# Kernel optimization log

Hardware: AMD Instinct MI355X
Metric: run time of the kernel (lower is better)

## Reference

```python
import jax, jax.numpy as jnp
import numpy as np


def setup_inputs() -> dict:
    key = jax.random.key(0)
    k1, k2, k3, k4 = jax.random.split(key, 4)
    B, L, R, H, D = 64, 512, 512, 512, 256
    return {
        "lstm_lt": jax.random.normal(k1, (B, L, H), dtype=jnp.float32),
        "lstm_rt": jax.random.normal(k2, (B, R, H), dtype=jnp.float32),
        "atten_W": jax.random.normal(k3, (H, D), dtype=jnp.float32) * 0.05,
        "diagnoal_W": jax.random.normal(k4, (1, 1, D), dtype=jnp.float32) * 0.05,
    }


def reference(lstm_lt, lstm_rt, atten_W, diagnoal_W):
    # Projection (the original's broadcast-multiply-sum is exactly a GEMM):
    # atten_lt[b,l,d] = tanh(sum_h lstm_lt[b,l,h] * W[h,d]) * diag_W[d]
    atten_lt = jnp.tanh(jnp.einsum('blh,hd->bld', lstm_lt, atten_W)) * diagnoal_W
    atten_rt = jnp.tanh(jnp.einsum('brh,hd->brd', lstm_rt, atten_W))
    # batch_dot over the attention dim -> (B, L, R)
    atten_value = jnp.einsum('bld,brd->blr', atten_lt, atten_rt)
    # No masks supplied (len(inputs)==2 path); softmax over last axis.
    return jax.nn.softmax(atten_value, axis=-1)
```

## Files before the change

kernel.cpp:

```cpp
#include <hip/hip_runtime.h>

typedef __attribute__((ext_vector_type(8))) __bf16 bf16x8;
typedef __attribute__((ext_vector_type(4))) float f32x4;

#define DI __device__ __forceinline__

DI unsigned short f2bf(float x) {
  unsigned u = __float_as_uint(x);
  u += 0x7fffu + ((u >> 16) & 1u);
  return (unsigned short)(u >> 16);
}

DI bf16x8 cvt8(f32x4 lo, f32x4 hi) {
  bf16x8 r;
  r[0] = (__bf16)lo.x; r[1] = (__bf16)lo.y; r[2] = (__bf16)lo.z; r[3] = (__bf16)lo.w;
  r[4] = (__bf16)hi.x; r[5] = (__bf16)hi.y; r[6] = (__bf16)hi.z; r[7] = (__bf16)hi.w;
  return r;
}

DI float tanh_fast(float x) {
  float ax = fabsf(x);
  float e = __expf(-2.0f * ax);
  float t = (1.0f - e) / (1.0f + e);
  return x < 0.0f ? -t : t;
}


__global__ void k_wt(const float* __restrict__ W, unsigned short* __restrict__ Wt) {
  int n  = blockIdx.x;
  int k8 = threadIdx.x;
  unsigned v[8];
#pragma unroll
  for (int j = 0; j < 8; j++) v[j] = f2bf(W[(k8 * 8 + j) * 256 + n]);
  uint4 p;
  p.x = v[0] | (v[1] << 16);
  p.y = v[2] | (v[3] << 16);
  p.z = v[4] | (v[5] << 16);
  p.w = v[6] | (v[7] << 16);
  size_t idx = ((size_t)(n >> 4) * 16 + (k8 >> 2)) * 512 + (k8 & 3) * 128 + (n & 15) * 8;
  *(uint4*)&Wt[idx] = p;
}

__global__ __launch_bounds__(512, 2) void k_proj(
    const float* __restrict__ Alt, const float* __restrict__ Art,
    const unsigned short* __restrict__ Wt, const float* __restrict__ diag,
    unsigned short* __restrict__ Olt, unsigned short* __restrict__ Ort) {
  int bx = blockIdx.x;
  bool is_lt = bx < 256;
  int m0 = (is_lt ? bx : bx - 256) * 128;
  const char* Abase = (const char*)((is_lt ? Alt : Art) + (size_t)m0 * 512);
  const char* Bt = (const char*)Wt;
  unsigned short* O = is_lt ? Olt : Ort;

  int tid  = threadIdx.x;
  int lane = tid & 63;
  int wid  = tid >> 6;
  int wm   = wid >> 2;
  int wn   = wid & 3;
  int l15  = lane & 15;
  int quad = lane >> 4;

  f32x4 zero = {0.0f, 0.0f, 0.0f, 0.0f};
  f32x4 acc[4][4];
#pragma unroll
  for (int i = 0; i < 4; i++)
#pragma unroll
    for (int j = 0; j < 4; j++) acc[i][j] = zero;

  const char* Arow = Abase + (size_t)(wm * 64 + l15) * 2048 + quad * 32;

#pragma unroll 2
  for (int t = 0; t < 8; t++) {
    uint4 bv[2][4];
#pragma unroll
    for (int ks = 0; ks < 2; ks++)
#pragma unroll
      for (int nt = 0; nt < 4; nt++)
        bv[ks][nt] = *(const uint4*)(
            Bt + (((size_t)(wn * 4 + nt) * 16 + t * 2 + ks) << 10) + lane * 16);

    bf16x8 a[2][4];
#pragma unroll
    for (int ks = 0; ks < 2; ks++)
#pragma unroll
      for (int mt = 0; mt < 4; mt++) {
        const char* ap = Arow + (size_t)mt * 32768 + t * 256 + ks * 128;
        f32x4 lo = *(const f32x4*)(ap);
        f32x4 hi = *(const f32x4*)(ap + 16);
        a[ks][mt] = cvt8(lo, hi);
      }

#pragma unroll
    for (int ks = 0; ks < 2; ks++)
#pragma unroll
      for (int mt = 0; mt < 4; mt++)
#pragma unroll
        for (int nt = 0; nt < 4; nt++)
          acc[mt][nt] = __builtin_amdgcn_mfma_f32_16x16x32_bf16(
              a[ks][mt], __builtin_bit_cast(bf16x8, bv[ks][nt]), acc[mt][nt], 0, 0, 0);
  }

  float dscale[4];
#pragma unroll
  for (int nt = 0; nt < 4; nt++)
    dscale[nt] = is_lt ? diag[wn * 64 + nt * 16 + l15] : 1.0f;

#pragma unroll
  for (int mt = 0; mt < 4; mt++)
#pragma unroll
    for (int r = 0; r < 4; r++) {
      int m = m0 + wm * 64 + mt * 16 + quad * 4 + r;
      int bb = m >> 9, rr = m & 511;
#pragma unroll
      for (int nt = 0; nt < 4; nt++) {
        int d = wn * 64 + nt * 16 + l15;
        size_t idx = (size_t)bb * 131072 +
                     ((size_t)(rr >> 4) * 8 + (d >> 5)) * 512 +
                     ((d >> 3) & 3) * 128 + (rr & 15) * 8 + (d & 7);
        O[idx] = f2bf(tanh_fast(acc[mt][nt][r]) * dscale[nt]);
      }
    }
}

__global__ __launch_bounds__(512, 4) void k_attn(
    const unsigned short* __restrict__ Lt, const unsigned short* __restrict__ Rt,
    float* __restrict__ Out) {
  __shared__ float red[8][64];
  __shared__ float rowv[64];

  int bx = blockIdx.x;
  int b  = (bx & 7) * 8 + ((bx >> 3) & 7);
  int l0 = (bx >> 6) * 64;
  const char* Lb = (const char*)Lt + (size_t)b * 262144;
  const char* Rb = (const char*)Rt + (size_t)b * 262144;
  float* Ob = Out + ((size_t)b * 512 + l0) * 512;

  int tid  = threadIdx.x;
  int lane = tid & 63;
  int wid  = tid >> 6;
  int l15  = lane & 15;
  int quad = lane >> 4;

  f32x4 zero = {0.0f, 0.0f, 0.0f, 0.0f};
  f32x4 acc[4][4];
#pragma unroll
  for (int i = 0; i < 4; i++)
#pragma unroll
    for (int j = 0; j < 4; j++) acc[i][j] = zero;

  int lrow = l0 >> 4;

  for (int t = 0; t < 8; t++) {
    uint4 av[4], rv[4];
#pragma unroll
    for (int mt = 0; mt < 4; mt++)
      av[mt] = *(const uint4*)(Lb + (((size_t)(lrow + mt) * 8 + t) << 10) + lane * 16);
#pragma unroll
    for (int nt = 0; nt < 4; nt++)
      rv[nt] = *(const uint4*)(Rb + (((size_t)(wid * 4 + nt) * 8 + t) << 10) + lane * 16);
#pragma unroll
    for (int mt = 0; mt < 4; mt++)
#pragma unroll
      for (int nt = 0; nt < 4; nt++)
        acc[mt][nt] = __builtin_amdgcn_mfma_f32_16x16x32_bf16(
            __builtin_bit_cast(bf16x8, av[mt]),
            __builtin_bit_cast(bf16x8, rv[nt]), acc[mt][nt], 0, 0, 0);
  }

#pragma unroll
  for (int mt = 0; mt < 4; mt++) {
#pragma unroll
    for (int r = 0; r < 4; r++) {
      float m = fmaxf(fmaxf(acc[mt][0][r], acc[mt][1][r]),
                      fmaxf(acc[mt][2][r], acc[mt][3][r]));
      m = fmaxf(m, __shfl_xor(m, 1));
      m = fmaxf(m, __shfl_xor(m, 2));
      m = fmaxf(m, __shfl_xor(m, 4));
      m = fmaxf(m, __shfl_xor(m, 8));
      if (l15 == 0) red[wid][mt * 16 + quad * 4 + r] = m;
    }
  }
  __syncthreads();
  if (tid < 64) {
    float m = red[0][tid];
#pragma unroll
    for (int w = 1; w < 8; w++) m = fmaxf(m, red[w][tid]);
    rowv[tid] = m;
  }
  __syncthreads();

#pragma unroll
  for (int mt = 0; mt < 4; mt++) {
#pragma unroll
    for (int r = 0; r < 4; r++) {
      float base = rowv[mt * 16 + quad * 4 + r];
      float s = 0.0f;
#pragma unroll
      for (int nt = 0; nt < 4; nt++) {
        float e = __expf(acc[mt][nt][r] - base);
        acc[mt][nt][r] = e;
        s += e;
      }
      s += __shfl_xor(s, 1);
      s += __shfl_xor(s, 2);
      s += __shfl_xor(s, 4);
      s += __shfl_xor(s, 8);
      if (l15 == 0) red[wid][mt * 16 + quad * 4 + r] = s;
    }
  }
  __syncthreads();
  if (tid < 64) {
    float s = red[0][tid];
#pragma unroll
    for (int w = 1; w < 8; w++) s += red[w][tid];
    rowv[tid] = 1.0f / s;
  }
  __syncthreads();

#pragma unroll
  for (int mt = 0; mt < 4; mt++) {
#pragma unroll
    for (int r = 0; r < 4; r++) {
      int row = mt * 16 + quad * 4 + r;
      float inv = rowv[row];
#pragma unroll
      for (int nt = 0; nt < 4; nt++) {
        int col = wid * 64 + nt * 16 + l15;
        Ob[(size_t)row * 512 + col] = acc[mt][nt][r] * inv;
      }
    }
  }
}

extern "C" void kernel_launch(void* const* d_in, const int* in_sizes, int n_in,
                              void* d_out, int out_size, void* d_ws, size_t ws_size,
                              hipStream_t stream) {
  const float* lstm_lt = (const float*)d_in[0];
  const float* lstm_rt = (const float*)d_in[1];
  const float* W       = (const float*)d_in[2];
  const float* diag    = (const float*)d_in[3];
  float* out = (float*)d_out;

  unsigned short* Wt  = (unsigned short*)d_ws;
  unsigned short* Olt = (unsigned short*)((char*)d_ws + (size_t)256 * 512 * 2);
  unsigned short* Ort = Olt + (size_t)32768 * 256;

  k_wt<<<dim3(256), dim3(64), 0, stream>>>(W, Wt);
  k_proj<<<dim3(512), dim3(512), 0, stream>>>(lstm_lt, lstm_rt, Wt, diag, Olt, Ort);
  k_attn<<<dim3(512), dim3(512), 0, stream>>>(Olt, Ort, out);
}
```

Before: 257.7 us.

## Stage projection A tiles through swizzled LDS with double-buffered prefetch

The projection kernel now covers 256 rows per block instead of 128. Each block cooperatively loads fp32 A rows with coalesced loads, converts them to bf16 and stores them in an XOR-swizzled, double-buffered LDS tile. Global loads for the next K step are issued before compute and barriers, so they overlap with the MFMA work, and MFMA sections run at raised wave priority. The cost is twice the accumulator registers (8x4 tiles), 64KB of LDS, and half as many blocks, which may reduce occupancy and latency hiding.

```diff
diff --git a/kernel.cpp b/kernel.cpp
--- a/kernel.cpp
+++ b/kernel.cpp
@@ -23,6 +23,17 @@
   float e = __expf(-2.0f * ax);
   float t = (1.0f - e) / (1.0f + e);
   return x < 0.0f ? -t : t;
+}
+
+DI void barx() {
+  __builtin_amdgcn_sched_barrier(0);
+  __builtin_amdgcn_s_barrier();
+  __builtin_amdgcn_sched_barrier(0);
+}
+DI void lgkm0() {
+  __builtin_amdgcn_sched_barrier(0);
+  asm volatile("s_waitcnt lgkmcnt(0)" ::: "memory");
+  __builtin_amdgcn_sched_barrier(0);
 }
 
 
@@ -45,9 +56,11 @@
     const float* __restrict__ Alt, const float* __restrict__ Art,
     const unsigned short* __restrict__ Wt, const float* __restrict__ diag,
     unsigned short* __restrict__ Olt, unsigned short* __restrict__ Ort) {
+  __shared__ __align__(16) unsigned short As[2][256 * 64];
+
   int bx = blockIdx.x;
-  bool is_lt = bx < 256;
-  int m0 = (is_lt ? bx : bx - 256) * 128;
+  bool is_lt = bx < 128;
+  int m0 = (is_lt ? bx : bx - 128) * 256;
   const char* Abase = (const char*)((is_lt ? Alt : Art) + (size_t)m0 * 512);
   const char* Bt = (const char*)Wt;
   unsigned short* O = is_lt ? Olt : Ort;
@@ -59,45 +72,87 @@
   int wn   = wid & 3;
   int l15  = lane & 15;
   int quad = lane >> 4;
+  int r7   = l15 & 7;
+
+  int srow  = tid >> 1;
+  int soff  = (tid & 1) * 128;
+  int cbase = (tid & 1) * 4;
 
   f32x4 zero = {0.0f, 0.0f, 0.0f, 0.0f};
-  f32x4 acc[4][4];
-#pragma unroll
-  for (int i = 0; i < 4; i++)
+  f32x4 acc[8][4];
+#pragma unroll
+  for (int i = 0; i < 8; i++)
 #pragma unroll
     for (int j = 0; j < 4; j++) acc[i][j] = zero;
 
-  const char* Arow = Abase + (size_t)(wm * 64 + l15) * 2048 + quad * 32;
-
-#pragma unroll 2
-  for (int t = 0; t < 8; t++) {
-    uint4 bv[2][4];
+  f32x4 av[8];
+  uint4 b0[2][4], b1[2][4];
+
+  auto issueA = [&](int t) {
+    const char* ap = Abase + (size_t)srow * 2048 + t * 256 + soff;
+#pragma unroll
+    for (int i = 0; i < 8; i++) av[i] = *(const f32x4*)(ap + i * 16);
+  };
+  auto issueB = [&](int t, uint4 (&b)[2][4]) {
 #pragma unroll
     for (int ks = 0; ks < 2; ks++)
 #pragma unroll
       for (int nt = 0; nt < 4; nt++)
-        bv[ks][nt] = *(const uint4*)(
+        b[ks][nt] = *(const uint4*)(
             Bt + (((size_t)(wn * 4 + nt) * 16 + t * 2 + ks) << 10) + lane * 16);
-
-    bf16x8 a[2][4];
-#pragma unroll
-    for (int ks = 0; ks < 2; ks++)
-#pragma unroll
-      for (int mt = 0; mt < 4; mt++) {
-        const char* ap = Arow + (size_t)mt * 32768 + t * 256 + ks * 128;
-        f32x4 lo = *(const f32x4*)(ap);
-        f32x4 hi = *(const f32x4*)(ap + 16);
-        a[ks][mt] = cvt8(lo, hi);
+  };
+  auto writeA = [&](int buf) {
+    char* AsB = (char*)&As[buf][0];
+#pragma unroll
+    for (int i = 0; i < 4; i++) {
+      int c = cbase + i;
+      *(bf16x8*)(AsB + srow * 128 + ((c ^ (srow & 7)) << 4)) =
+          cvt8(av[i * 2], av[i * 2 + 1]);
+    }
+  };
+  auto compute = [&](int buf, uint4 (&b)[2][4]) {
+    const char* AsB = (const char*)&As[buf][0];
+#pragma unroll
+    for (int ks = 0; ks < 2; ks++) {
+      bf16x8 a[8];
+#pragma unroll
+      for (int mt = 0; mt < 8; mt++) {
+        int row = wm * 128 + mt * 16 + l15;
+        a[mt] = *(const bf16x8*)(AsB + row * 128 + (((ks * 4 + quad) ^ r7) << 4));
       }
-
-#pragma unroll
-    for (int ks = 0; ks < 2; ks++)
-#pragma unroll
-      for (int mt = 0; mt < 4; mt++)
+      __builtin_amdgcn_s_setprio(1);
+#pragma unroll
+      for (int mt = 0; mt < 8; mt++)
 #pragma unroll
         for (int nt = 0; nt < 4; nt++)
           acc[mt][nt] = __builtin_amdgcn_mfma_f32_16x16x32_bf16(
-              a[ks][mt], __builtin_bit_cast(bf16x8, bv[ks][nt]), acc[mt][nt], 0, 0, 0);
+              a[mt], __builtin_bit_cast(bf16x8, b[ks][nt]), acc[mt][nt], 0, 0, 0);
+      __builtin_amdgcn_s_setprio(0);
+    }
+  };
+
+  issueA(0);
+  issueB(0, b0);
+  writeA(0);
+  issueA(1);
+  issueB(1, b1);
+  lgkm0();
+  barx();
+
+#pragma unroll
+  for (int t = 0; t < 8; t += 2) {
+    compute(0, b0);
+    writeA(1);
+    if (t < 6) { issueA(t + 2); issueB(t + 2, b0); }
+    lgkm0();
+    barx();
+    compute(1, b1);
+    if (t < 6) {
+      writeA(0);
+      issueA(t + 3); issueB(t + 3, b1);
+      lgkm0();
+      barx();
+    }
   }
 
   float dscale[4];
@@ -106,10 +161,10 @@
     dscale[nt] = is_lt ? diag[wn * 64 + nt * 16 + l15] : 1.0f;
 
 #pragma unroll
-  for (int mt = 0; mt < 4; mt++)
+  for (int mt = 0; mt < 8; mt++)
 #pragma unroll
     for (int r = 0; r < 4; r++) {
-      int m = m0 + wm * 64 + mt * 16 + quad * 4 + r;
+      int m = m0 + wm * 128 + mt * 16 + quad * 4 + r;
       int bb = m >> 9, rr = m & 511;
 #pragma unroll
       for (int nt = 0; nt < 4; nt++) {
@@ -246,6 +301,6 @@
   unsigned short* Ort = Olt + (size_t)32768 * 256;
 
   k_wt<<<dim3(256), dim3(64), 0, stream>>>(W, Wt);
-  k_proj<<<dim3(512), dim3(512), 0, stream>>>(lstm_lt, lstm_rt, Wt, diag, Olt, Ort);
+  k_proj<<<dim3(256), dim3(512), 0, stream>>>(lstm_lt, lstm_rt, Wt, diag, Olt, Ort);
   k_attn<<<dim3(512), dim3(512), 0, stream>>>(Olt, Ort, out);
 }
```

After: 255.2 us. Within noise of the previous version (-1.0%).
